# Performance work log

Hardware: AMD Instinct MI355X
Metric: run time of the kernel (lower is better)

The kernel has to match this reference:

```python
import jax, jax.numpy as jnp
import numpy as np

B, D, C = 32, 30, 4        # batch, input spatial, in-channels
KS = 3                     # kernel size per dim
OD = D - KS + 1            # 28 (valid padding, stride 1)
P = OD ** 3                # 21952 output positions
K = (KS ** 3) * C          # 108 taps per output position
F = 4                      # output filters


def _patches(x):
    # x: [B, D, D, D, C] -> [B, P, K]
    xt = jnp.transpose(x, (0, 4, 1, 2, 3))  # NCDHW
    p = jax.lax.conv_general_dilated_patches(
        xt, filter_shape=(KS, KS, KS), window_strides=(1, 1, 1), padding='VALID')
    # p: [B, C*KS^3, OD, OD, OD]
    p = jnp.transpose(p, (0, 2, 3, 4, 1))
    return p.reshape(p.shape[0], P, K)


def _local_conv(x, W):
    # Locally-connected 3D conv (unshared weights) == structured sparse matmul.
    # W: [P, K, F] one weight per (output position, tap, filter).
    return jnp.einsum('bpk,pkf->bpf', _patches(x), W)


def setup_inputs() -> dict:
    key = jax.random.key(0)
    ks = jax.random.split(key, 7)
    x = jax.random.normal(ks[0], (B, D, D, D, C), jnp.float32)
    kernel_loc = jax.random.normal(ks[1], (P, K, F), jnp.float32) * 0.05
    kernel_rho = jax.random.normal(ks[2], (P, K, F), jnp.float32) * 0.1 - 5.0  # softplus -> small scale
    bias = jax.random.normal(ks[3], (F,), jnp.float32) * 0.05
    eps = jax.random.normal(ks[4], (P, K, F), jnp.float32)
    sign_in = jax.random.rademacher(ks[5], (B, D, D, D, C), jnp.float32)
    sign_out = jax.random.rademacher(ks[6], (B, P, F), jnp.float32)
    return dict(x=x, kernel_loc=kernel_loc, kernel_rho=kernel_rho, bias=bias,
                eps=eps, sign_in=sign_in, sign_out=sign_out)


def reference(x, kernel_loc, kernel_rho, bias, eps, sign_in, sign_out):
    # Flipout estimator: deterministic mean path + sign-perturbed noise path.
    scale = jax.nn.softplus(kernel_rho)
    out = _local_conv(x, kernel_loc)                                  # [B, P, F]
    out = out + sign_out * _local_conv(x * sign_in, scale * eps)      # flipout perturbation
    out = out + bias                                                  # per-filter bias (channels_last)
    return out.reshape(x.shape[0], OD, OD, OD, F)
```

## Files before the change

### kernel.cpp

```cpp
#include <hip/hip_runtime.h>


constexpr int Bn   = 32;
constexpr int Dn   = 30;
constexpr int Cn   = 4;
constexpr int ODn  = 28;
constexpr int Pn   = ODn * ODn * ODn;
constexpr int Tt   = 27;
constexpr int Kn   = Tt * Cn;
constexpr int PPB  = 16;
constexpr int NT   = Pn / PPB;
constexpr int THREADS = 256;
constexpr int WSTRIDE = Kn + 1;
constexpr int GRID = NT;

__device__ __forceinline__ unsigned bf16rne(float f) {
    unsigned u = __float_as_uint(f);
    return (u + 0x7fffu + ((u >> 16) & 1u)) >> 16;
}
__device__ __forceinline__ float bflo(unsigned u) { return __uint_as_float(u << 16); }
__device__ __forceinline__ float bfhi(unsigned u) { return __uint_as_float(u & 0xffff0000u); }

__global__ __launch_bounds__(THREADS) void lc3d_flipout_kernel(
    const float* __restrict__ x,
    const float* __restrict__ loc,
    const float* __restrict__ rho,
    const float* __restrict__ bias,
    const float* __restrict__ eps,
    const float* __restrict__ sgn_in,
    const float* __restrict__ sgn_out,
    float* __restrict__ out)
{
    __shared__ uint4 wsh[PPB * WSTRIDE];

    const int tid = threadIdx.x;

    const int xcd  = blockIdx.x & 7;
    const int slot = blockIdx.x >> 3;
    const int Tx = (xcd < 4) ? xcd * 172 : 688 + (xcd - 4) * 171;
    const int p_base = (Tx + slot) * PPB;

    const float4* loc4 = (const float4*)loc + (size_t)p_base * Kn;
    const float4* rho4 = (const float4*)rho + (size_t)p_base * Kn;
    const float4* eps4 = (const float4*)eps + (size_t)p_base * Kn;
    for (int g = tid; g < PPB * Kn; g += THREADS) {
        const int plc = g / Kn;
        const int k   = g - plc * Kn;
        const float4 L = loc4[g];
        const float4 R = rho4[g];
        const float4 E = eps4[g];
        float nx = (R.x > 15.f ? R.x : __logf(1.f + __expf(R.x))) * E.x;
        float ny = (R.y > 15.f ? R.y : __logf(1.f + __expf(R.y))) * E.y;
        float nz = (R.z > 15.f ? R.z : __logf(1.f + __expf(R.z))) * E.z;
        float nw = (R.w > 15.f ? R.w : __logf(1.f + __expf(R.w))) * E.w;
        uint4 pk;
        pk.x = bf16rne(L.x) | (bf16rne(L.y) << 16);
        pk.y = bf16rne(L.z) | (bf16rne(L.w) << 16);
        pk.z = bf16rne(nx)  | (bf16rne(ny) << 16);
        pk.w = bf16rne(nz)  | (bf16rne(nw) << 16);
        wsh[plc * WSTRIDE + k] = pk;
    }
    __syncthreads();

    const int pl = tid & 15;
    const int bh = tid >> 4;
    const int b0 = bh, b1 = bh + 16;
    const int p  = p_base + pl;
    const int od = p / (ODn * ODn);
    const int prem = p - od * (ODn * ODn);
    const int oh = prem / ODn;
    const int ow = prem - oh * ODn;
    const float4* x4 = (const float4*)x;
    const float4* s4 = (const float4*)sgn_in;
    const size_t v0 = (((size_t)b0 * Dn + od) * Dn + oh) * Dn + ow;
    const size_t v1 = (((size_t)b1 * Dn + od) * Dn + oh) * Dn + ow;
    const uint4* wp = wsh + pl * WSTRIDE;

    float a00=0.f,a01=0.f,a02=0.f,a03=0.f, a10=0.f,a11=0.f,a12=0.f,a13=0.f;
    float n00=0.f,n01=0.f,n02=0.f,n03=0.f, n10=0.f,n11=0.f,n12=0.f,n13=0.f;

#define CHAN(c, xa_c, sa_c, xb_c, sb_c)                                      \
    {                                                                        \
        const uint4 wv = wp[(c) * Tt + t];                                   \
        const float m0 = bflo(wv.x), m1 = bfhi(wv.x);                        \
        const float m2 = bflo(wv.y), m3 = bfhi(wv.y);                        \
        const float q0 = bflo(wv.z), q1 = bfhi(wv.z);                        \
        const float q2 = bflo(wv.w), q3 = bfhi(wv.w);                        \
        a00 = fmaf(xa_c, m0, a00); a01 = fmaf(xa_c, m1, a01);                \
        a02 = fmaf(xa_c, m2, a02); a03 = fmaf(xa_c, m3, a03);                \
        a10 = fmaf(xb_c, m0, a10); a11 = fmaf(xb_c, m1, a11);                \
        a12 = fmaf(xb_c, m2, a12); a13 = fmaf(xb_c, m3, a13);                \
        const float ya = (xa_c) * (sa_c);                                    \
        const float yb = (xb_c) * (sb_c);                                    \
        n00 = fmaf(ya, q0, n00); n01 = fmaf(ya, q1, n01);                    \
        n02 = fmaf(ya, q2, n02); n03 = fmaf(ya, q3, n03);                    \
        n10 = fmaf(yb, q0, n10); n11 = fmaf(yb, q1, n11);                    \
        n12 = fmaf(yb, q2, n12); n13 = fmaf(yb, q3, n13);                    \
    }

    #pragma unroll
    for (int kd = 0; kd < 3; ++kd) {
        #pragma unroll
        for (int kh = 0; kh < 3; ++kh) {
            const int roff = (kd * Dn + kh) * Dn;
            #pragma unroll
            for (int kw = 0; kw < 3; ++kw) {
                const int t = (kd * 3 + kh) * 3 + kw;
                const float4 xa = x4[v0 + roff + kw];
                const float4 sa = s4[v0 + roff + kw];
                const float4 xb = x4[v1 + roff + kw];
                const float4 sb = s4[v1 + roff + kw];
                CHAN(0, xa.x, sa.x, xb.x, sb.x);
                CHAN(1, xa.y, sa.y, xb.y, sb.y);
                CHAN(2, xa.z, sa.z, xb.z, sb.z);
                CHAN(3, xa.w, sa.w, xb.w, sb.w);
            }
        }
    }
#undef CHAN

    const float4 bi = *(const float4*)bias;
    const size_t ob0 = (size_t)b0 * Pn + p;
    const size_t ob1 = (size_t)b1 * Pn + p;
    const float4 so0 = ((const float4*)sgn_out)[ob0];
    const float4 so1 = ((const float4*)sgn_out)[ob1];
    float4 o0, o1;
    o0.x = fmaf(so0.x, n00, a00) + bi.x;
    o0.y = fmaf(so0.y, n01, a01) + bi.y;
    o0.z = fmaf(so0.z, n02, a02) + bi.z;
    o0.w = fmaf(so0.w, n03, a03) + bi.w;
    o1.x = fmaf(so1.x, n10, a10) + bi.x;
    o1.y = fmaf(so1.y, n11, a11) + bi.y;
    o1.z = fmaf(so1.z, n12, a12) + bi.z;
    o1.w = fmaf(so1.w, n13, a13) + bi.w;
    ((float4*)out)[ob0] = o0;
    ((float4*)out)[ob1] = o1;
}

extern "C" void kernel_launch(void* const* d_in, const int* in_sizes, int n_in,
                              void* d_out, int out_size, void* d_ws, size_t ws_size,
                              hipStream_t stream) {
    const float* x    = (const float*)d_in[0];
    const float* loc  = (const float*)d_in[1];
    const float* rho  = (const float*)d_in[2];
    const float* bias = (const float*)d_in[3];
    const float* eps  = (const float*)d_in[4];
    const float* si   = (const float*)d_in[5];
    const float* so   = (const float*)d_in[6];
    float* out = (float*)d_out;

    lc3d_flipout_kernel<<<dim3(GRID), dim3(THREADS), 0, stream>>>(
        x, loc, rho, bias, eps, si, so, out);
}
```

Measured before the change: 212.3 us.

## Use 512 threads with one batch per thread and batched weight staging loads

The block grows to 512 threads, and each thread now computes a single batch element instead of two, which halves the per-thread accumulators and doubles the thread-level parallelism. The weight-staging loop is replaced by explicit straight-line loads: three float4 triples are issued up front and a tail handles the remaining entries, so more loads are in flight before softplus and packing. In exchange, each shared-memory weight read is reused across fewer batches per thread, so LDS traffic per FMA doubles. Occupancy per CU may also shift with the larger block.

```diff
diff --git a/kernel.cpp b/kernel.cpp
--- a/kernel.cpp
+++ b/kernel.cpp
@@ -10,7 +10,7 @@
 constexpr int Kn   = Tt * Cn;
 constexpr int PPB  = 16;
 constexpr int NT   = Pn / PPB;
-constexpr int THREADS = 256;
+constexpr int THREADS = 512;
 constexpr int WSTRIDE = Kn + 1;
 constexpr int GRID = NT;
 
@@ -20,6 +20,19 @@
 }
 __device__ __forceinline__ float bflo(unsigned u) { return __uint_as_float(u << 16); }
 __device__ __forceinline__ float bfhi(unsigned u) { return __uint_as_float(u & 0xffff0000u); }
+
+__device__ __forceinline__ uint4 pack_w(const float4 L, const float4 R, const float4 E) {
+    float nx = (R.x > 15.f ? R.x : __logf(1.f + __expf(R.x))) * E.x;
+    float ny = (R.y > 15.f ? R.y : __logf(1.f + __expf(R.y))) * E.y;
+    float nz = (R.z > 15.f ? R.z : __logf(1.f + __expf(R.z))) * E.z;
+    float nw = (R.w > 15.f ? R.w : __logf(1.f + __expf(R.w))) * E.w;
+    uint4 pk;
+    pk.x = bf16rne(L.x) | (bf16rne(L.y) << 16);
+    pk.y = bf16rne(L.z) | (bf16rne(L.w) << 16);
+    pk.z = bf16rne(nx)  | (bf16rne(ny) << 16);
+    pk.w = bf16rne(nz)  | (bf16rne(nw) << 16);
+    return pk;
+}
 
 __global__ __launch_bounds__(THREADS) void lc3d_flipout_kernel(
     const float* __restrict__ x,
@@ -40,31 +53,36 @@
     const int Tx = (xcd < 4) ? xcd * 172 : 688 + (xcd - 4) * 171;
     const int p_base = (Tx + slot) * PPB;
 
-    const float4* loc4 = (const float4*)loc + (size_t)p_base * Kn;
-    const float4* rho4 = (const float4*)rho + (size_t)p_base * Kn;
-    const float4* eps4 = (const float4*)eps + (size_t)p_base * Kn;
-    for (int g = tid; g < PPB * Kn; g += THREADS) {
-        const int plc = g / Kn;
-        const int k   = g - plc * Kn;
-        const float4 L = loc4[g];
-        const float4 R = rho4[g];
-        const float4 E = eps4[g];
-        float nx = (R.x > 15.f ? R.x : __logf(1.f + __expf(R.x))) * E.x;
-        float ny = (R.y > 15.f ? R.y : __logf(1.f + __expf(R.y))) * E.y;
-        float nz = (R.z > 15.f ? R.z : __logf(1.f + __expf(R.z))) * E.z;
-        float nw = (R.w > 15.f ? R.w : __logf(1.f + __expf(R.w))) * E.w;
-        uint4 pk;
-        pk.x = bf16rne(L.x) | (bf16rne(L.y) << 16);
-        pk.y = bf16rne(L.z) | (bf16rne(L.w) << 16);
-        pk.z = bf16rne(nx)  | (bf16rne(ny) << 16);
-        pk.w = bf16rne(nz)  | (bf16rne(nw) << 16);
-        wsh[plc * WSTRIDE + k] = pk;
+    {
+        const float4* loc4 = (const float4*)loc + (size_t)p_base * Kn;
+        const float4* rho4 = (const float4*)rho + (size_t)p_base * Kn;
+        const float4* eps4 = (const float4*)eps + (size_t)p_base * Kn;
+        const int g0 = tid, g1 = tid + 512, g2 = tid + 1024;
+        const float4 L0 = loc4[g0], R0 = rho4[g0], E0 = eps4[g0];
+        const float4 L1 = loc4[g1], R1 = rho4[g1], E1 = eps4[g1];
+        const float4 L2 = loc4[g2], R2 = rho4[g2], E2 = eps4[g2];
+        {
+            const int plc = g0 / Kn, k = g0 - plc * Kn;
+            wsh[plc * WSTRIDE + k] = pack_w(L0, R0, E0);
+        }
+        {
+            const int plc = g1 / Kn, k = g1 - plc * Kn;
+            wsh[plc * WSTRIDE + k] = pack_w(L1, R1, E1);
+        }
+        {
+            const int plc = g2 / Kn, k = g2 - plc * Kn;
+            wsh[plc * WSTRIDE + k] = pack_w(L2, R2, E2);
+        }
+        if (tid < PPB * Kn - 1536) {
+            const int g3 = tid + 1536;
+            const int plc = g3 / Kn, k = g3 - plc * Kn;
+            wsh[plc * WSTRIDE + k] = pack_w(loc4[g3], rho4[g3], eps4[g3]);
+        }
     }
     __syncthreads();
 
     const int pl = tid & 15;
-    const int bh = tid >> 4;
-    const int b0 = bh, b1 = bh + 16;
+    const int b  = tid >> 4;
     const int p  = p_base + pl;
     const int od = p / (ODn * ODn);
     const int prem = p - od * (ODn * ODn);
@@ -72,30 +90,23 @@
     const int ow = prem - oh * ODn;
     const float4* x4 = (const float4*)x;
     const float4* s4 = (const float4*)sgn_in;
-    const size_t v0 = (((size_t)b0 * Dn + od) * Dn + oh) * Dn + ow;
-    const size_t v1 = (((size_t)b1 * Dn + od) * Dn + oh) * Dn + ow;
+    const size_t v0 = (((size_t)b * Dn + od) * Dn + oh) * Dn + ow;
     const uint4* wp = wsh + pl * WSTRIDE;
 
-    float a00=0.f,a01=0.f,a02=0.f,a03=0.f, a10=0.f,a11=0.f,a12=0.f,a13=0.f;
-    float n00=0.f,n01=0.f,n02=0.f,n03=0.f, n10=0.f,n11=0.f,n12=0.f,n13=0.f;
+    float a0=0.f,a1=0.f,a2=0.f,a3=0.f, n0=0.f,n1=0.f,n2=0.f,n3=0.f;
 
-#define CHAN(c, xa_c, sa_c, xb_c, sb_c)                                      \
+#define CHAN(c, x_c, s_c)                                                    \
     {                                                                        \
         const uint4 wv = wp[(c) * Tt + t];                                   \
         const float m0 = bflo(wv.x), m1 = bfhi(wv.x);                        \
         const float m2 = bflo(wv.y), m3 = bfhi(wv.y);                        \
         const float q0 = bflo(wv.z), q1 = bfhi(wv.z);                        \
         const float q2 = bflo(wv.w), q3 = bfhi(wv.w);                        \
-        a00 = fmaf(xa_c, m0, a00); a01 = fmaf(xa_c, m1, a01);                \
-        a02 = fmaf(xa_c, m2, a02); a03 = fmaf(xa_c, m3, a03);                \
-        a10 = fmaf(xb_c, m0, a10); a11 = fmaf(xb_c, m1, a11);                \
-        a12 = fmaf(xb_c, m2, a12); a13 = fmaf(xb_c, m3, a13);                \
-        const float ya = (xa_c) * (sa_c);                                    \
-        const float yb = (xb_c) * (sb_c);                                    \
-        n00 = fmaf(ya, q0, n00); n01 = fmaf(ya, q1, n01);                    \
-        n02 = fmaf(ya, q2, n02); n03 = fmaf(ya, q3, n03);                    \
-        n10 = fmaf(yb, q0, n10); n11 = fmaf(yb, q1, n11);                    \
-        n12 = fmaf(yb, q2, n12); n13 = fmaf(yb, q3, n13);                    \
+        a0 = fmaf(x_c, m0, a0); a1 = fmaf(x_c, m1, a1);                      \
+        a2 = fmaf(x_c, m2, a2); a3 = fmaf(x_c, m3, a3);                      \
+        const float ya = (x_c) * (s_c);                                      \
+        n0 = fmaf(ya, q0, n0); n1 = fmaf(ya, q1, n1);                        \
+        n2 = fmaf(ya, q2, n2); n3 = fmaf(ya, q3, n3);                        \
     }
 
     #pragma unroll
@@ -108,33 +119,24 @@
                 const int t = (kd * 3 + kh) * 3 + kw;
                 const float4 xa = x4[v0 + roff + kw];
                 const float4 sa = s4[v0 + roff + kw];
-                const float4 xb = x4[v1 + roff + kw];
-                const float4 sb = s4[v1 + roff + kw];
-                CHAN(0, xa.x, sa.x, xb.x, sb.x);
-                CHAN(1, xa.y, sa.y, xb.y, sb.y);
-                CHAN(2, xa.z, sa.z, xb.z, sb.z);
-                CHAN(3, xa.w, sa.w, xb.w, sb.w);
+                CHAN(0, xa.x, sa.x);
+                CHAN(1, xa.y, sa.y);
+                CHAN(2, xa.z, sa.z);
+                CHAN(3, xa.w, sa.w);
             }
         }
     }
 #undef CHAN
 
     const float4 bi = *(const float4*)bias;
-    const size_t ob0 = (size_t)b0 * Pn + p;
-    const size_t ob1 = (size_t)b1 * Pn + p;
-    const float4 so0 = ((const float4*)sgn_out)[ob0];
-    const float4 so1 = ((const float4*)sgn_out)[ob1];
-    float4 o0, o1;
-    o0.x = fmaf(so0.x, n00, a00) + bi.x;
-    o0.y = fmaf(so0.y, n01, a01) + bi.y;
-    o0.z = fmaf(so0.z, n02, a02) + bi.z;
-    o0.w = fmaf(so0.w, n03, a03) + bi.w;
-    o1.x = fmaf(so1.x, n10, a10) + bi.x;
-    o1.y = fmaf(so1.y, n11, a11) + bi.y;
-    o1.z = fmaf(so1.z, n12, a12) + bi.z;
-    o1.w = fmaf(so1.w, n13, a13) + bi.w;
-    ((float4*)out)[ob0] = o0;
-    ((float4*)out)[ob1] = o1;
+    const size_t ob = (size_t)b * Pn + p;
+    const float4 so = ((const float4*)sgn_out)[ob];
+    float4 o;
+    o.x = fmaf(so.x, n0, a0) + bi.x;
+    o.y = fmaf(so.y, n1, a1) + bi.y;
+    o.z = fmaf(so.z, n2, a2) + bi.z;
+    o.w = fmaf(so.w, n3, a3) + bi.w;
+    ((float4*)out)[ob] = o;
 }
 
 extern "C" void kernel_launch(void* const* d_in, const int* in_sizes, int n_in,
```

After: 206.1 us. -2.9%, faster.

## Remap threads to two adjacent positions per batch and unroll weight staging

Applied to the files above, without the earlier changes.

Each thread now handles two neighbouring output positions for a single batch instead of one position for two batches. Overlapping input windows can then be shared: each tap row loads four x/sign vectors instead of six, and the sign multiply is done once per loaded voxel. The weight staging loop is also manually unrolled so several global loads are in flight at once. The cost is twice as many LDS weight reads per tap, since the two positions use different unshared weights.

```diff
diff --git a/kernel.cpp b/kernel.cpp
--- a/kernel.cpp
+++ b/kernel.cpp
@@ -21,6 +21,19 @@
 __device__ __forceinline__ float bflo(unsigned u) { return __uint_as_float(u << 16); }
 __device__ __forceinline__ float bfhi(unsigned u) { return __uint_as_float(u & 0xffff0000u); }
 
+__device__ __forceinline__ uint4 pack_w(const float4 L, const float4 R, const float4 E) {
+    float nx = (R.x > 15.f ? R.x : __logf(1.f + __expf(R.x))) * E.x;
+    float ny = (R.y > 15.f ? R.y : __logf(1.f + __expf(R.y))) * E.y;
+    float nz = (R.z > 15.f ? R.z : __logf(1.f + __expf(R.z))) * E.z;
+    float nw = (R.w > 15.f ? R.w : __logf(1.f + __expf(R.w))) * E.w;
+    uint4 pk;
+    pk.x = bf16rne(L.x) | (bf16rne(L.y) << 16);
+    pk.y = bf16rne(L.z) | (bf16rne(L.w) << 16);
+    pk.z = bf16rne(nx)  | (bf16rne(ny) << 16);
+    pk.w = bf16rne(nz)  | (bf16rne(nw) << 16);
+    return pk;
+}
+
 __global__ __launch_bounds__(THREADS) void lc3d_flipout_kernel(
     const float* __restrict__ x,
     const float* __restrict__ loc,
@@ -40,90 +53,110 @@
     const int Tx = (xcd < 4) ? xcd * 172 : 688 + (xcd - 4) * 171;
     const int p_base = (Tx + slot) * PPB;
 
-    const float4* loc4 = (const float4*)loc + (size_t)p_base * Kn;
-    const float4* rho4 = (const float4*)rho + (size_t)p_base * Kn;
-    const float4* eps4 = (const float4*)eps + (size_t)p_base * Kn;
-    for (int g = tid; g < PPB * Kn; g += THREADS) {
-        const int plc = g / Kn;
-        const int k   = g - plc * Kn;
-        const float4 L = loc4[g];
-        const float4 R = rho4[g];
-        const float4 E = eps4[g];
-        float nx = (R.x > 15.f ? R.x : __logf(1.f + __expf(R.x))) * E.x;
-        float ny = (R.y > 15.f ? R.y : __logf(1.f + __expf(R.y))) * E.y;
-        float nz = (R.z > 15.f ? R.z : __logf(1.f + __expf(R.z))) * E.z;
-        float nw = (R.w > 15.f ? R.w : __logf(1.f + __expf(R.w))) * E.w;
-        uint4 pk;
-        pk.x = bf16rne(L.x) | (bf16rne(L.y) << 16);
-        pk.y = bf16rne(L.z) | (bf16rne(L.w) << 16);
-        pk.z = bf16rne(nx)  | (bf16rne(ny) << 16);
-        pk.w = bf16rne(nz)  | (bf16rne(nw) << 16);
-        wsh[plc * WSTRIDE + k] = pk;
+    {
+        const float4* loc4 = (const float4*)loc + (size_t)p_base * Kn;
+        const float4* rho4 = (const float4*)rho + (size_t)p_base * Kn;
+        const float4* eps4 = (const float4*)eps + (size_t)p_base * Kn;
+#define STG2(ga, gb)                                                         \
+        {                                                                    \
+            const int g0 = tid + (ga), g1 = tid + (gb);                      \
+            const float4 La = loc4[g0], Ra = rho4[g0], Ea = eps4[g0];        \
+            const float4 Lb = loc4[g1], Rb = rho4[g1], Eb = eps4[g1];        \
+            { const int p_ = g0 / Kn, k_ = g0 - p_ * Kn;                     \
+              wsh[p_ * WSTRIDE + k_] = pack_w(La, Ra, Ea); }                 \
+            { const int p_ = g1 / Kn, k_ = g1 - p_ * Kn;                     \
+              wsh[p_ * WSTRIDE + k_] = pack_w(Lb, Rb, Eb); }                 \
+        }
+        STG2(0, 256)
+        STG2(512, 768)
+        STG2(1024, 1280)
+        if (tid < PPB * Kn - 1536) {
+            const int g = tid + 1536;
+            const int p_ = g / Kn, k_ = g - p_ * Kn;
+            wsh[p_ * WSTRIDE + k_] = pack_w(loc4[g], rho4[g], eps4[g]);
+        }
+#undef STG2
     }
     __syncthreads();
 
-    const int pl = tid & 15;
-    const int bh = tid >> 4;
-    const int b0 = bh, b1 = bh + 16;
-    const int p  = p_base + pl;
-    const int od = p / (ODn * ODn);
-    const int prem = p - od * (ODn * ODn);
+    const int j = tid & 7;
+    const int b = tid >> 3;
+    const int p0 = p_base + 2 * j;
+    const int od = p0 / (ODn * ODn);
+    const int prem = p0 - od * (ODn * ODn);
     const int oh = prem / ODn;
     const int ow = prem - oh * ODn;
     const float4* x4 = (const float4*)x;
     const float4* s4 = (const float4*)sgn_in;
-    const size_t v0 = (((size_t)b0 * Dn + od) * Dn + oh) * Dn + ow;
-    const size_t v1 = (((size_t)b1 * Dn + od) * Dn + oh) * Dn + ow;
-    const uint4* wp = wsh + pl * WSTRIDE;
+    const size_t v0 = (((size_t)b * Dn + od) * Dn + oh) * Dn + ow;
+    const uint4* wp0 = wsh + (2 * j) * WSTRIDE;
+    const uint4* wp1 = wp0 + WSTRIDE;
 
-    float a00=0.f,a01=0.f,a02=0.f,a03=0.f, a10=0.f,a11=0.f,a12=0.f,a13=0.f;
-    float n00=0.f,n01=0.f,n02=0.f,n03=0.f, n10=0.f,n11=0.f,n12=0.f,n13=0.f;
+    float a00=0.f,a01=0.f,a02=0.f,a03=0.f, n00=0.f,n01=0.f,n02=0.f,n03=0.f;
+    float a10=0.f,a11=0.f,a12=0.f,a13=0.f, n10=0.f,n11=0.f,n12=0.f,n13=0.f;
 
-#define CHAN(c, xa_c, sa_c, xb_c, sb_c)                                      \
+#define CH1(c, t, xa, ya, xb, yb)                                            \
     {                                                                        \
-        const uint4 wv = wp[(c) * Tt + t];                                   \
-        const float m0 = bflo(wv.x), m1 = bfhi(wv.x);                        \
-        const float m2 = bflo(wv.y), m3 = bfhi(wv.y);                        \
-        const float q0 = bflo(wv.z), q1 = bfhi(wv.z);                        \
-        const float q2 = bflo(wv.w), q3 = bfhi(wv.w);                        \
-        a00 = fmaf(xa_c, m0, a00); a01 = fmaf(xa_c, m1, a01);                \
-        a02 = fmaf(xa_c, m2, a02); a03 = fmaf(xa_c, m3, a03);                \
-        a10 = fmaf(xb_c, m0, a10); a11 = fmaf(xb_c, m1, a11);                \
-        a12 = fmaf(xb_c, m2, a12); a13 = fmaf(xb_c, m3, a13);                \
-        const float ya = (xa_c) * (sa_c);                                    \
-        const float yb = (xb_c) * (sb_c);                                    \
-        n00 = fmaf(ya, q0, n00); n01 = fmaf(ya, q1, n01);                    \
-        n02 = fmaf(ya, q2, n02); n03 = fmaf(ya, q3, n03);                    \
-        n10 = fmaf(yb, q0, n10); n11 = fmaf(yb, q1, n11);                    \
-        n12 = fmaf(yb, q2, n12); n13 = fmaf(yb, q3, n13);                    \
+        const uint4 w0 = wp0[(c) * Tt + (t)];                                \
+        const uint4 w1 = wp1[(c) * Tt + (t)];                                \
+        a00 = fmaf(xa, bflo(w0.x), a00); a01 = fmaf(xa, bfhi(w0.x), a01);    \
+        a02 = fmaf(xa, bflo(w0.y), a02); a03 = fmaf(xa, bfhi(w0.y), a03);    \
+        n00 = fmaf(ya, bflo(w0.z), n00); n01 = fmaf(ya, bfhi(w0.z), n01);    \
+        n02 = fmaf(ya, bflo(w0.w), n02); n03 = fmaf(ya, bfhi(w0.w), n03);    \
+        a10 = fmaf(xb, bflo(w1.x), a10); a11 = fmaf(xb, bfhi(w1.x), a11);    \
+        a12 = fmaf(xb, bflo(w1.y), a12); a13 = fmaf(xb, bfhi(w1.y), a13);    \
+        n10 = fmaf(yb, bflo(w1.z), n10); n11 = fmaf(yb, bfhi(w1.z), n11);    \
+        n12 = fmaf(yb, bflo(w1.w), n12); n13 = fmaf(yb, bfhi(w1.w), n13);    \
+    }
+
+#define KWC(kd, kh, kw, XA, YA, XB, YB)                                      \
+    {                                                                        \
+        const int t = ((kd) * 3 + (kh)) * 3 + (kw);                          \
+        CH1(0, t, XA.x, YA.x, XB.x, YB.x)                                    \
+        CH1(1, t, XA.y, YA.y, XB.y, YB.y)                                    \
+        CH1(2, t, XA.z, YA.z, XB.z, YB.z)                                    \
+        CH1(3, t, XA.w, YA.w, XB.w, YB.w)                                    \
+    }
+
+#define TAPROW(kd, kh)                                                       \
+    {                                                                        \
+        const int roff = ((kd) * Dn + (kh)) * Dn;                            \
+        const float4 X0 = x4[v0 + roff + 0];                                 \
+        const float4 X1 = x4[v0 + roff + 1];                                 \
+        const float4 X2 = x4[v0 + roff + 2];                                 \
+        const float4 X3 = x4[v0 + roff + 3];                                 \
+        const float4 S0 = s4[v0 + roff + 0];                                 \
+        const float4 S1 = s4[v0 + roff + 1];                                 \
+        const float4 S2 = s4[v0 + roff + 2];                                 \
+        const float4 S3 = s4[v0 + roff + 3];                                 \
+        float4 Y0, Y1, Y2, Y3;                                               \
+        Y0.x = X0.x * S0.x; Y0.y = X0.y * S0.y;                              \
+        Y0.z = X0.z * S0.z; Y0.w = X0.w * S0.w;                              \
+        Y1.x = X1.x * S1.x; Y1.y = X1.y * S1.y;                              \
+        Y1.z = X1.z * S1.z; Y1.w = X1.w * S1.w;                              \
+        Y2.x = X2.x * S2.x; Y2.y = X2.y * S2.y;                              \
+        Y2.z = X2.z * S2.z; Y2.w = X2.w * S2.w;                              \
+        Y3.x = X3.x * S3.x; Y3.y = X3.y * S3.y;                              \
+        Y3.z = X3.z * S3.z; Y3.w = X3.w * S3.w;                              \
+        KWC(kd, kh, 0, X0, Y0, X1, Y1)                                       \
+        KWC(kd, kh, 1, X1, Y1, X2, Y2)                                       \
+        KWC(kd, kh, 2, X2, Y2, X3, Y3)                                       \
     }
 
     #pragma unroll
     for (int kd = 0; kd < 3; ++kd) {
-        #pragma unroll
-        for (int kh = 0; kh < 3; ++kh) {
-            const int roff = (kd * Dn + kh) * Dn;
-            #pragma unroll
-            for (int kw = 0; kw < 3; ++kw) {
-                const int t = (kd * 3 + kh) * 3 + kw;
-                const float4 xa = x4[v0 + roff + kw];
-                const float4 sa = s4[v0 + roff + kw];
-                const float4 xb = x4[v1 + roff + kw];
-                const float4 sb = s4[v1 + roff + kw];
-                CHAN(0, xa.x, sa.x, xb.x, sb.x);
-                CHAN(1, xa.y, sa.y, xb.y, sb.y);
-                CHAN(2, xa.z, sa.z, xb.z, sb.z);
-                CHAN(3, xa.w, sa.w, xb.w, sb.w);
-            }
-        }
+        TAPROW(kd, 0)
+        TAPROW(kd, 1)
+        TAPROW(kd, 2)
     }
-#undef CHAN
+#undef TAPROW
+#undef KWC
+#undef CH1
 
     const float4 bi = *(const float4*)bias;
-    const size_t ob0 = (size_t)b0 * Pn + p;
-    const size_t ob1 = (size_t)b1 * Pn + p;
+    const size_t ob0 = (size_t)b * Pn + p0;
     const float4 so0 = ((const float4*)sgn_out)[ob0];
-    const float4 so1 = ((const float4*)sgn_out)[ob1];
+    const float4 so1 = ((const float4*)sgn_out)[ob0 + 1];
     float4 o0, o1;
     o0.x = fmaf(so0.x, n00, a00) + bi.x;
     o0.y = fmaf(so0.y, n01, a01) + bi.y;
@@ -133,8 +166,8 @@
     o1.y = fmaf(so1.y, n11, a11) + bi.y;
     o1.z = fmaf(so1.z, n12, a12) + bi.z;
     o1.w = fmaf(so1.w, n13, a13) + bi.w;
-    ((float4*)out)[ob0] = o0;
-    ((float4*)out)[ob1] = o1;
+    ((float4*)out)[ob0]     = o0;
+    ((float4*)out)[ob0 + 1] = o1;
 }
 
 extern "C" void kernel_launch(void* const* d_in, const int* in_sizes, int n_in,
```

New measurement: 248.4 us. 17.0% more time.
